# Kernel optimization log

Hardware: AMD Instinct MI355X
Metric: run time of the kernel (lower is better)

## Reference

```python
import jax, jax.numpy as jnp
import numpy as np

NUM_Q_HEADS = 16
NUM_KV_HEADS = 4
GROUP_SIZE = NUM_Q_HEADS // NUM_KV_HEADS  # 4
GROUP_DIM = 128                           # head dim, also RoPE dim
THETA = 10000.0


def _rope_cos_sin(num_tokens, dim, dtype):
    # freqs = 1/theta^(2i/d); angles[t, i] = t * freqs[i]
    inv_freq = 1.0 / (THETA ** (jnp.arange(0, dim, 2, dtype=jnp.float32) / dim))
    t = jnp.arange(num_tokens, dtype=jnp.float32)
    angles = jnp.outer(t, inv_freq)  # [N, d/2]
    # broadcast to [N, 1, 1, d/2] to match q/k shape [B, N, gs, kvh, d/2]
    cos = jnp.cos(angles)[:, None, None, :].astype(dtype)
    sin = jnp.sin(angles)[:, None, None, :].astype(dtype)
    return cos, sin


def _apply_rope(x, cos, sin):
    # x: [B, N, gs, kvh, d]; complex rotation on interleaved (even, odd) pairs
    xr = x.reshape(*x.shape[:-1], -1, 2)
    xe, xo = xr[..., 0], xr[..., 1]
    oe = xe * cos - xo * sin
    oo = xe * sin + xo * cos
    return jnp.stack([oe, oo], axis=-1).reshape(x.shape)


def setup_inputs() -> dict:
    key = jax.random.key(0)
    ks = jax.random.split(key, 5)
    B, N, D = 1, 2048, 2048
    KV_D = GROUP_DIM * NUM_KV_HEADS  # 512
    s = 0.02
    return {
        "x": jax.random.normal(ks[0], (B, N, D), dtype=jnp.float32),
        "Wq": jax.random.normal(ks[1], (D, D), dtype=jnp.float32) * s,
        "Wk": jax.random.normal(ks[2], (D, KV_D), dtype=jnp.float32) * s,
        "Wv": jax.random.normal(ks[3], (D, KV_D), dtype=jnp.float32) * s,
        "Wo": jax.random.normal(ks[4], (D, D), dtype=jnp.float32) * s,
    }


def reference(x, Wq, Wk, Wv, Wo):
    B, N, D = x.shape
    d = GROUP_DIM
    # projections
    q = (x @ Wq).reshape(B, N, GROUP_SIZE, NUM_KV_HEADS, d)
    k = (x @ Wk).reshape(B, N, 1, NUM_KV_HEADS, d)
    v = (x @ Wv).reshape(B, N, 1, NUM_KV_HEADS, d)
    # RoPE (interleaved complex rotation)
    cos, sin = _rope_cos_sin(N, d, x.dtype)
    q = _apply_rope(q, cos, sin)
    k = _apply_rope(k, cos, sin)
    # to [B, kvh, gs, N, d] / [B, kvh, N, d]
    q = jnp.transpose(q, (0, 3, 2, 1, 4))        # b k s n d
    k = jnp.transpose(k[:, :, 0], (0, 2, 1, 3))  # b k m d
    v = jnp.transpose(v[:, :, 0], (0, 2, 1, 3))  # b k m d
    scores = jnp.einsum('bksnd,bkmd->bksnm', q, k)
    causal = jnp.tril(jnp.ones((N, N), dtype=bool))
    scores = jnp.where(causal, scores, -jnp.inf)
    weights = jax.nn.softmax(scores / jnp.sqrt(jnp.asarray(d, x.dtype)), axis=-1)
    ctx = jnp.einsum('bksnm,bkmd->bksnd', weights, v)   # [B, kvh, gs, N, d]
    # flatten heads (kvh-major, matching torch flatten(1,2)), then [B, N, D]
    ctx = ctx.reshape(B, NUM_KV_HEADS * GROUP_SIZE, N, d)
    ctx = jnp.transpose(ctx, (0, 2, 1, 3)).reshape(B, N, D)
    return ctx @ Wo
```

## Files before the change

### kernel.cpp

```cpp
#include <hip/hip_runtime.h>

typedef unsigned short u16;
typedef float f32x4 __attribute__((ext_vector_type(4)));
typedef short s16x8 __attribute__((ext_vector_type(8)));
typedef short s16x4 __attribute__((ext_vector_type(4)));

__device__ __forceinline__ u16 f2b(float f) {
  union { float f; unsigned u; } v; v.f = f;
  unsigned r = v.u + 0x7fffu + ((v.u >> 16) & 1u);
  return (u16)(r >> 16);
}
__device__ __forceinline__ float b2f(u16 b) {
  union { unsigned u; float f; } v; v.u = ((unsigned)b) << 16;
  return v.f;
}
__device__ __forceinline__ f32x4 mfma_bf16(s16x8 a, s16x8 b, f32x4 c) {
  return __builtin_amdgcn_mfma_f32_16x16x32_bf16(a, b, c, 0, 0, 0);
}
__device__ __forceinline__ void gl_lds16(const u16* g, u16* l) {
  __builtin_amdgcn_global_load_lds(
      (const __attribute__((address_space(1))) void*)g,
      (__attribute__((address_space(3))) void*)l, 16, 0, 0);
}

__global__ void conv_x(const float* __restrict__ in, u16* __restrict__ out, int n) {
  int i = (blockIdx.x * 256 + threadIdx.x) * 8;
  if (i >= n) return;
  f32x4 a = *(const f32x4*)(in + i);
  f32x4 b = *(const f32x4*)(in + i + 4);
  s16x8 o = {(short)f2b(a.x), (short)f2b(a.y), (short)f2b(a.z), (short)f2b(a.w),
             (short)f2b(b.x), (short)f2b(b.y), (short)f2b(b.z), (short)f2b(b.w)};
  *(s16x8*)(out + i) = o;
}

__global__ void transW(const float* __restrict__ Wq, const float* __restrict__ Wk,
                       const float* __restrict__ Wv, const float* __restrict__ Wo,
                       u16* __restrict__ WqkvT, u16* __restrict__ WoT) {
  __shared__ u16 tile[64][68];
  const int z = blockIdx.z;
  if (z == 1 && blockIdx.x >= 32) return;
  const int ox = blockIdx.x * 64;
  const int oy = blockIdx.y * 64;
  const float* src; int scol, C; u16* dst;
  if (z == 0) {
    if (ox < 2048)      { src = Wq; scol = ox;        C = 2048; }
    else if (ox < 2560) { src = Wk; scol = ox - 2048; C = 512;  }
    else                { src = Wv; scol = ox - 2560; C = 512;  }
    dst = WqkvT;
  } else { src = Wo; scol = ox; C = 2048; dst = WoT; }
  const int t = threadIdx.x, lr = t >> 4, c4 = (t & 15) * 4;
#pragma unroll
  for (int p = 0; p < 4; ++p) {
    int r = p * 16 + lr;
    f32x4 v = *(const f32x4*)(src + (size_t)(oy + r) * C + scol + c4);
    s16x4 pk = {(short)f2b(v.x), (short)f2b(v.y), (short)f2b(v.z), (short)f2b(v.w)};
    *(s16x4*)(&tile[r][c4]) = pk;
  }
  __syncthreads();
#pragma unroll
  for (int q = 0; q < 4; ++q) {
    int oc = q * 16 + lr;
    s16x4 pk = {(short)tile[c4 + 0][oc], (short)tile[c4 + 1][oc],
                (short)tile[c4 + 2][oc], (short)tile[c4 + 3][oc]};
    *(s16x4*)(dst + (size_t)(ox + oc) * 2048 + oy + c4) = pk;
  }
}

__global__ void transpose_v(const u16* __restrict__ qkv, u16* __restrict__ vT) {
  __shared__ u16 tile[64][68];
  const int bx = blockIdx.x * 64;
  const int by = blockIdx.y * 64;
  const int t = threadIdx.x, lr = t >> 4, c4 = (t & 15) * 4;
#pragma unroll
  for (int p = 0; p < 4; ++p) {
    int r = p * 16 + lr;
    s16x4 v = *(const s16x4*)(qkv + (size_t)(by + r) * 3072 + 2560 + bx + c4);
    *(s16x4*)(&tile[r][c4]) = v;
  }
  __syncthreads();
#pragma unroll
  for (int q = 0; q < 4; ++q) {
    int oc = q * 16 + lr;
    s16x4 pk = {(short)tile[c4 + 0][oc], (short)tile[c4 + 1][oc],
                (short)tile[c4 + 2][oc], (short)tile[c4 + 3][oc]};
    *(s16x4*)(vT + (size_t)(bx + oc) * 2048 + by + c4) = pk;
  }
}

__global__ __launch_bounds__(256, 2) void gemm_qkv(const u16* __restrict__ A,
                                                   const u16* __restrict__ Bt,
                                                   u16* __restrict__ C) {
  __shared__ __align__(16) u16 As[64 * 32];
  __shared__ __align__(16) u16 Bs[128 * 32];
  const int K = 2048;
  const int n0 = blockIdx.x * 128, m0 = blockIdx.y * 64;
  const int t = threadIdx.x, wave = t >> 6, lane = t & 63;
  const int quad = lane >> 4, lc = lane & 15;
  const int wm = (wave >> 1) * 32, wn = (wave & 1) * 64;
  const int arow = t >> 2, akc = (t & 3) * 8;

  const f32x4 z = {0.f, 0.f, 0.f, 0.f};
  f32x4 acc[2][4];
#pragma unroll
  for (int i = 0; i < 2; ++i)
#pragma unroll
    for (int j = 0; j < 4; ++j) acc[i][j] = z;

  for (int k0 = 0; k0 < K; k0 += 32) {
    gl_lds16(A  + (size_t)(m0 + arow) * K + k0 + akc, As + wave * 512);
    gl_lds16(Bt + (size_t)(n0 + arow) * K + k0 + akc, Bs + wave * 512);
    gl_lds16(Bt + (size_t)(n0 + 64 + arow) * K + k0 + akc, Bs + 2048 + wave * 512);
    __syncthreads();
    s16x8 af[2], bfr[4];
#pragma unroll
    for (int i = 0; i < 2; ++i)
      af[i] = *(const s16x8*)(As + (wm + i * 16 + lc) * 32 + quad * 8);
#pragma unroll
    for (int j = 0; j < 4; ++j)
      bfr[j] = *(const s16x8*)(Bs + (wn + j * 16 + lc) * 32 + quad * 8);
#pragma unroll
    for (int i = 0; i < 2; ++i)
#pragma unroll
      for (int j = 0; j < 4; ++j)
        acc[i][j] = mfma_bf16(af[i], bfr[j], acc[i][j]);
    __syncthreads();
  }
#pragma unroll
  for (int j = 0; j < 4; ++j) {
    const int colbase = wn + j * 16;
    const bool rope = (n0 + colbase) < 2560;
    const int col = n0 + colbase + lc;
    const int ip = ((colbase + lc) & 127) >> 1;
    const float inv_freq = exp2f(-0.20762050593046014f * (float)ip);
#pragma unroll
    for (int i = 0; i < 2; ++i)
#pragma unroll
      for (int r = 0; r < 4; ++r) {
        float v = acc[i][j][r];
        float p = __shfl_xor(v, 1);
        float val = v;
        if (rope) {
          int token = m0 + wm + i * 16 + quad * 4 + r;
          float ang = (float)token * inv_freq;
          float sv, cv;
          sincosf(ang, &sv, &cv);
          val = (lc & 1) ? (p * sv + v * cv) : (v * cv - p * sv);
        }
        C[(size_t)(m0 + wm + i * 16 + quad * 4 + r) * 3072 + col] = f2b(val);
      }
  }
}

__global__ __launch_bounds__(256, 2) void gemm_out(const u16* __restrict__ A,
                                                   const u16* __restrict__ Bt,
                                                   float* __restrict__ C) {
  __shared__ __align__(16) u16 As[64 * 32];
  __shared__ __align__(16) u16 Bs[128 * 32];
  const int K = 2048;
  const int n0 = blockIdx.x * 128, m0 = blockIdx.y * 64;
  const int t = threadIdx.x, wave = t >> 6, lane = t & 63;
  const int quad = lane >> 4, lc = lane & 15;
  const int wm = (wave >> 1) * 32, wn = (wave & 1) * 64;
  const int arow = t >> 2, akc = (t & 3) * 8;

  const f32x4 z = {0.f, 0.f, 0.f, 0.f};
  f32x4 acc[2][4];
#pragma unroll
  for (int i = 0; i < 2; ++i)
#pragma unroll
    for (int j = 0; j < 4; ++j) acc[i][j] = z;

  for (int k0 = 0; k0 < K; k0 += 32) {
    gl_lds16(A  + (size_t)(m0 + arow) * K + k0 + akc, As + wave * 512);
    gl_lds16(Bt + (size_t)(n0 + arow) * K + k0 + akc, Bs + wave * 512);
    gl_lds16(Bt + (size_t)(n0 + 64 + arow) * K + k0 + akc, Bs + 2048 + wave * 512);
    __syncthreads();
    s16x8 af[2], bfr[4];
#pragma unroll
    for (int i = 0; i < 2; ++i)
      af[i] = *(const s16x8*)(As + (wm + i * 16 + lc) * 32 + quad * 8);
#pragma unroll
    for (int j = 0; j < 4; ++j)
      bfr[j] = *(const s16x8*)(Bs + (wn + j * 16 + lc) * 32 + quad * 8);
#pragma unroll
    for (int i = 0; i < 2; ++i)
#pragma unroll
      for (int j = 0; j < 4; ++j)
        acc[i][j] = mfma_bf16(af[i], bfr[j], acc[i][j]);
    __syncthreads();
  }
#pragma unroll
  for (int i = 0; i < 2; ++i)
#pragma unroll
    for (int j = 0; j < 4; ++j)
#pragma unroll
      for (int r = 0; r < 4; ++r)
        C[(size_t)(m0 + wm + i * 16 + quad * 4 + r) * 2048 + n0 + wn + j * 16 + lc] =
            acc[i][j][r];
}

__global__ __launch_bounds__(256, 2) void attn_k(const u16* __restrict__ qkv,
                                                 const u16* __restrict__ vT,
                                                 u16* __restrict__ Opart,
                                                 float* __restrict__ Lpart) {
  const int qt = blockIdx.x, hq = blockIdx.y, half = blockIdx.z;
  const int kvh = hq & 3, sg = hq >> 2;
  const int qc0 = hq << 7, kc0 = 2048 + (kvh << 7), vr0 = kvh << 7;

  __shared__ __align__(16) u16 Qs[64 * 136];
  __shared__ __align__(16) u16 KVs[128 * 72];
  __shared__ __align__(16) u16 Ps[64 * 72];

  const int t = threadIdx.x, wave = t >> 6, lane = t & 63;
  const int quad = lane >> 4, lc = lane & 15;

  {
    int r = t >> 4, cc = (t & 15) * 8;
#pragma unroll
    for (int pass = 0; pass < 4; ++pass) {
      int row = pass * 16 + r;
      *(s16x8*)(Qs + row * 136 + cc) =
          *(const s16x8*)(qkv + (size_t)(qt * 64 + row) * 3072 + qc0 + cc);
    }
  }

  const f32x4 z = {0.f, 0.f, 0.f, 0.f};
  f32x4 oa[8];
#pragma unroll
  for (int n = 0; n < 8; ++n) oa[n] = z;
  float Ls[4] = {0.f, 0.f, 0.f, 0.f};
  const float scale = 0.08838834764831845f;
  const int qrow_base = qt * 64 + wave * 16 + quad * 4;

  const int ntiles = qt + 1, n0t = (ntiles + 1) >> 1;
  const int lo = half ? n0t : 0, hi = half ? ntiles : n0t;

  for (int tile = lo; tile < hi; ++tile) {
    const int j0 = tile * 64;
    __syncthreads();
    {
      int r = t >> 4, cc = (t & 15) * 8;
#pragma unroll
      for (int pass = 0; pass < 4; ++pass) {
        int row = pass * 16 + r;
        *(s16x8*)(KVs + row * 136 + cc) =
            *(const s16x8*)(qkv + (size_t)(j0 + row) * 3072 + kc0 + cc);
      }
    }
    __syncthreads();
    f32x4 sa[4];
#pragma unroll
    for (int n = 0; n < 4; ++n) sa[n] = z;
#pragma unroll
    for (int ks = 0; ks < 4; ++ks) {
      s16x8 af = *(const s16x8*)(Qs + (wave * 16 + lc) * 136 + ks * 32 + quad * 8);
#pragma unroll
      for (int n = 0; n < 4; ++n) {
        s16x8 bf = *(const s16x8*)(KVs + (n * 16 + lc) * 136 + ks * 32 + quad * 8);
        sa[n] = mfma_bf16(af, bf, sa[n]);
      }
    }
#pragma unroll
    for (int n = 0; n < 4; ++n) {
      int jc = j0 + n * 16 + lc;
#pragma unroll
      for (int r = 0; r < 4; ++r) {
        float e = (jc <= qrow_base + r) ? __expf(sa[n][r] * scale) : 0.f;
        Ps[(wave * 16 + quad * 4 + r) * 72 + n * 16 + lc] = f2b(e);
        Ls[r] += e;
      }
    }
    __syncthreads();
    {
      int r = t >> 3, cc = (t & 7) * 8;
#pragma unroll
      for (int pass = 0; pass < 4; ++pass) {
        int row = pass * 32 + r;
        *(s16x8*)(KVs + row * 72 + cc) =
            *(const s16x8*)(vT + (size_t)(vr0 + row) * 2048 + j0 + cc);
      }
    }
    __syncthreads();
#pragma unroll
    for (int ks = 0; ks < 2; ++ks) {
      s16x8 af = *(const s16x8*)(Ps + (wave * 16 + lc) * 72 + ks * 32 + quad * 8);
#pragma unroll
      for (int n = 0; n < 8; ++n) {
        s16x8 bf = *(const s16x8*)(KVs + (n * 16 + lc) * 72 + ks * 32 + quad * 8);
        oa[n] = mfma_bf16(af, bf, oa[n]);
      }
    }
  }
#pragma unroll
  for (int r = 0; r < 4; ++r) {
    float s = Ls[r];
    s += __shfl_xor(s, 1);
    s += __shfl_xor(s, 2);
    s += __shfl_xor(s, 4);
    s += __shfl_xor(s, 8);
    Ls[r] = s;
  }
  const size_t tbase = (size_t)(half * 16 + hq) * 32 + qt;
  u16* Ob = Opart + tbase * (64 * 128);
  if (lc == 0) {
#pragma unroll
    for (int r = 0; r < 4; ++r)
      Lpart[tbase * 64 + wave * 16 + quad * 4 + r] = Ls[r];
  }
#pragma unroll
  for (int n = 0; n < 8; ++n)
#pragma unroll
    for (int r = 0; r < 4; ++r)
      Ob[(wave * 16 + quad * 4 + r) * 128 + n * 16 + lc] = f2b(oa[n][r]);
}

__global__ void attn_combine(const u16* __restrict__ Opart,
                             const float* __restrict__ Lpart,
                             u16* __restrict__ ctx) {
  const int hq = blockIdx.y, kvh = hq & 3, sg = hq >> 2;
  const int lin = blockIdx.x * 256 + threadIdx.x;
  const int token = lin >> 4, d8 = (lin & 15) << 3;
  const int qt = token >> 6, row = token & 63;
  const size_t t0 = (size_t)hq * 32 + qt, t1 = t0 + 512;
  const u16* O0 = Opart + t0 * 8192 + row * 128 + d8;
  const u16* O1 = Opart + t1 * 8192 + row * 128 + d8;
  const float inv = 1.f / (Lpart[t0 * 64 + row] + Lpart[t1 * 64 + row]);
  s16x8 a = *(const s16x8*)O0, b = *(const s16x8*)O1;
  s16x8 o;
#pragma unroll
  for (int i = 0; i < 8; ++i)
    o[i] = (short)f2b((b2f((u16)a[i]) + b2f((u16)b[i])) * inv);
  *(s16x8*)(ctx + (size_t)token * 2048 + ((kvh * 4 + sg) << 7) + d8) = o;
}

extern "C" void kernel_launch(void* const* d_in, const int* in_sizes, int n_in,
                              void* d_out, int out_size, void* d_ws, size_t ws_size,
                              hipStream_t stream) {
  const float* x  = (const float*)d_in[0];
  const float* Wq = (const float*)d_in[1];
  const float* Wk = (const float*)d_in[2];
  const float* Wv = (const float*)d_in[3];
  const float* Wo = (const float*)d_in[4];

  char* w = (char*)d_ws;
  u16* xb     = (u16*)w;  w += (size_t)2048 * 2048 * 2;
  u16* WqkvT  = (u16*)w;  w += (size_t)3072 * 2048 * 2;
  u16* WoT    = (u16*)w;  w += (size_t)2048 * 2048 * 2;
  u16* qkvb   = (u16*)w;  w += (size_t)2048 * 3072 * 2;
  u16* vTb    = (u16*)w;  w += (size_t)512 * 2048 * 2;
  u16* ctxb   = (u16*)w;  w += (size_t)2048 * 2048 * 2;
  float* Lpart= (float*)w; w += (size_t)2 * 16 * 32 * 64 * 4;
  u16* Opart  = (u16*)d_ws;

  conv_x<<<2048, 256, 0, stream>>>(x, xb, 2048 * 2048);
  transW<<<dim3(48, 32, 2), 256, 0, stream>>>(Wq, Wk, Wv, Wo, WqkvT, WoT);

  gemm_qkv<<<dim3(24, 32), 256, 0, stream>>>(xb, WqkvT, qkvb);

  transpose_v<<<dim3(8, 32), 256, 0, stream>>>(qkvb, vTb);

  attn_k<<<dim3(32, 16, 2), 256, 0, stream>>>(qkvb, vTb, Opart, Lpart);
  attn_combine<<<dim3(128, 16), 256, 0, stream>>>(Opart, Lpart, ctxb);

  gemm_out<<<dim3(16, 32), 256, 0, stream>>>(ctxb, WoT, (float*)d_out);
}
```

Baseline: 266.3 us.

## Prefetch next K/V tile into registers and split K/V LDS buffers

The attention kernel now loads the next tile's K and V rows into registers while the current tile is being computed, then stores them into separate K and V shared-memory buffers at the top of the next iteration. Splitting the combined K/V buffer also removes the two extra barriers and the serialized V load between the QK and PV phases. The softmax exponent switches to exp2f with log2(e) folded into the scale constant. In exchange the kernel uses more LDS and about 32 extra VGPRs per thread, which may pressure occupancy under the 2-block launch bound.

Measured after the change: 263.1 us. About the same (-1.2%).

```diff
diff --git a/kernel.cpp b/kernel.cpp
--- a/kernel.cpp
+++ b/kernel.cpp
@@ -208,20 +208,20 @@
   const int qc0 = hq << 7, kc0 = 2048 + (kvh << 7), vr0 = kvh << 7;
 
   __shared__ __align__(16) u16 Qs[64 * 136];
-  __shared__ __align__(16) u16 KVs[128 * 72];
+  __shared__ __align__(16) u16 Ks[64 * 136];
+  __shared__ __align__(16) u16 Vs[128 * 72];
   __shared__ __align__(16) u16 Ps[64 * 72];
 
   const int t = threadIdx.x, wave = t >> 6, lane = t & 63;
   const int quad = lane >> 4, lc = lane & 15;
+  const int kr = t >> 4, kc = (t & 15) * 8;
+  const int vr = t >> 3, vc = (t & 7) * 8;
 
   {
-    int r = t >> 4, cc = (t & 15) * 8;
-#pragma unroll
-    for (int pass = 0; pass < 4; ++pass) {
-      int row = pass * 16 + r;
-      *(s16x8*)(Qs + row * 136 + cc) =
-          *(const s16x8*)(qkv + (size_t)(qt * 64 + row) * 3072 + qc0 + cc);
-    }
+#pragma unroll
+    for (int p = 0; p < 4; ++p)
+      *(s16x8*)(Qs + (p * 16 + kr) * 136 + kc) =
+          *(const s16x8*)(qkv + (size_t)(qt * 64 + p * 16 + kr) * 3072 + qc0 + kc);
   }
 
   const f32x4 z = {0.f, 0.f, 0.f, 0.f};
@@ -229,23 +229,40 @@
 #pragma unroll
   for (int n = 0; n < 8; ++n) oa[n] = z;
   float Ls[4] = {0.f, 0.f, 0.f, 0.f};
-  const float scale = 0.08838834764831845f;
+  const float scale2 = 0.12751744545f;
   const int qrow_base = qt * 64 + wave * 16 + quad * 4;
 
   const int ntiles = qt + 1, n0t = (ntiles + 1) >> 1;
   const int lo = half ? n0t : 0, hi = half ? ntiles : n0t;
 
+  s16x8 kreg[4], vreg[4];
+  if (lo < hi) {
+    const int j0 = lo * 64;
+#pragma unroll
+    for (int p = 0; p < 4; ++p)
+      kreg[p] = *(const s16x8*)(qkv + (size_t)(j0 + p * 16 + kr) * 3072 + kc0 + kc);
+#pragma unroll
+    for (int p = 0; p < 4; ++p)
+      vreg[p] = *(const s16x8*)(vT + (size_t)(vr0 + p * 32 + vr) * 2048 + j0 + vc);
+  }
+
   for (int tile = lo; tile < hi; ++tile) {
     const int j0 = tile * 64;
     __syncthreads();
-    {
-      int r = t >> 4, cc = (t & 15) * 8;
-#pragma unroll
-      for (int pass = 0; pass < 4; ++pass) {
-        int row = pass * 16 + r;
-        *(s16x8*)(KVs + row * 136 + cc) =
-            *(const s16x8*)(qkv + (size_t)(j0 + row) * 3072 + kc0 + cc);
-      }
+#pragma unroll
+    for (int p = 0; p < 4; ++p)
+      *(s16x8*)(Ks + (p * 16 + kr) * 136 + kc) = kreg[p];
+#pragma unroll
+    for (int p = 0; p < 4; ++p)
+      *(s16x8*)(Vs + (p * 32 + vr) * 72 + vc) = vreg[p];
+    if (tile + 1 < hi) {
+      const int j1 = j0 + 64;
+#pragma unroll
+      for (int p = 0; p < 4; ++p)
+        kreg[p] = *(const s16x8*)(qkv + (size_t)(j1 + p * 16 + kr) * 3072 + kc0 + kc);
+#pragma unroll
+      for (int p = 0; p < 4; ++p)
+        vreg[p] = *(const s16x8*)(vT + (size_t)(vr0 + p * 32 + vr) * 2048 + j1 + vc);
     }
     __syncthreads();
     f32x4 sa[4];
@@ -256,7 +273,7 @@
       s16x8 af = *(const s16x8*)(Qs + (wave * 16 + lc) * 136 + ks * 32 + quad * 8);
 #pragma unroll
       for (int n = 0; n < 4; ++n) {
-        s16x8 bf = *(const s16x8*)(KVs + (n * 16 + lc) * 136 + ks * 32 + quad * 8);
+        s16x8 bf = *(const s16x8*)(Ks + (n * 16 + lc) * 136 + ks * 32 + quad * 8);
         sa[n] = mfma_bf16(af, bf, sa[n]);
       }
     }
@@ -265,28 +282,17 @@
       int jc = j0 + n * 16 + lc;
 #pragma unroll
       for (int r = 0; r < 4; ++r) {
-        float e = (jc <= qrow_base + r) ? __expf(sa[n][r] * scale) : 0.f;
+        float e = (jc <= qrow_base + r) ? exp2f(sa[n][r] * scale2) : 0.f;
         Ps[(wave * 16 + quad * 4 + r) * 72 + n * 16 + lc] = f2b(e);
         Ls[r] += e;
       }
     }
-    __syncthreads();
-    {
-      int r = t >> 3, cc = (t & 7) * 8;
-#pragma unroll
-      for (int pass = 0; pass < 4; ++pass) {
-        int row = pass * 32 + r;
-        *(s16x8*)(KVs + row * 72 + cc) =
-            *(const s16x8*)(vT + (size_t)(vr0 + row) * 2048 + j0 + cc);
-      }
-    }
-    __syncthreads();
 #pragma unroll
     for (int ks = 0; ks < 2; ++ks) {
       s16x8 af = *(const s16x8*)(Ps + (wave * 16 + lc) * 72 + ks * 32 + quad * 8);
 #pragma unroll
       for (int n = 0; n < 8; ++n) {
-        s16x8 bf = *(const s16x8*)(KVs + (n * 16 + lc) * 72 + ks * 32 + quad * 8);
+        s16x8 bf = *(const s16x8*)(Vs + (n * 16 + lc) * 72 + ks * 32 + quad * 8);
         oa[n] = mfma_bf16(af, bf, oa[n]);
       }
     }
```
